# Kernel tuning notes

Hardware: AMD Instinct MI355X
Metric: run time of the kernel (lower is better)

Reference implementation:

```python
import jax, jax.numpy as jnp
import numpy as np

N = 50000      # nodes
E = 800000     # edges
F = 128        # node feature dim
H = 256        # hidden dim
A = 32         # action dim
G = 50         # graphs in batch
EPS = 1e-5     # batchnorm eps


def setup_inputs() -> dict:
    key = jax.random.key(0)
    ks = jax.random.split(key, 24)
    s = 0.02
    inp = {
        "x": jax.random.normal(ks[0], (N, F), jnp.float32),
        "edge_index": jax.random.randint(ks[1], (2, E), 0, N, jnp.int64),
        "batch": jnp.sort(jax.random.randint(ks[2], (N,), 0, G, jnp.int64)),
        "actions": jax.random.normal(ks[3], (A,), jnp.float32),
        # GCNConv weights (x @ W + b convention)
        "W1": jax.random.normal(ks[4], (F, H), jnp.float32) * s,
        "b1": jnp.zeros((H,), jnp.float32),
        "W2": jax.random.normal(ks[5], (H, H), jnp.float32) * s,
        "b2": jnp.zeros((H,), jnp.float32),
        "W3": jax.random.normal(ks[6], (H, H), jnp.float32) * s,
        "b3": jnp.zeros((H,), jnp.float32),
        # batchnorm affine params
        "g1": jnp.ones((H,), jnp.float32), "be1": jnp.zeros((H,), jnp.float32),
        "g2": jnp.ones((H,), jnp.float32), "be2": jnp.zeros((H,), jnp.float32),
        "g3": jnp.ones((H,), jnp.float32), "be3": jnp.zeros((H,), jnp.float32),
        # MLP head
        "fW1": jax.random.normal(ks[7], (H + A, H), jnp.float32) * s,
        "fb1": jnp.zeros((H,), jnp.float32),
        "fW2": jax.random.normal(ks[8], (H, H // 2), jnp.float32) * s,
        "fb2": jnp.zeros((H // 2,), jnp.float32),
        "fW3": jax.random.normal(ks[9], (H // 2, 1), jnp.float32) * s,
        "fb3": jnp.zeros((1,), jnp.float32),
    }
    return inp


def _batchnorm(h, gamma, beta):
    # training-mode batchnorm over the row dimension (biased variance, as torch)
    mu = h.mean(0)
    var = ((h - mu) ** 2).mean(0)
    return (h - mu) * jax.lax.rsqrt(var + EPS) * gamma + beta


def reference(x, edge_index, batch, actions,
              W1, b1, W2, b2, W3, b3,
              g1, be1, g2, be2, g3, be3,
              fW1, fb1, fW2, fb2, fW3, fb3):
    src, dst = edge_index[0], edge_index[1]
    n = x.shape[0]
    # GCN symmetric normalization with self-loops: deg_i = 1 + in_degree(i)
    deg = jnp.zeros((n,), x.dtype).at[dst].add(1.0) + 1.0
    dis = jax.lax.rsqrt(deg)                       # deg^{-1/2}
    enorm = dis[src] * dis[dst]                    # [E]
    self_norm = (dis * dis)[:, None]               # 1/deg_i for self-loop edge

    def gcn(h, W, b):
        h = h @ W                                  # [n,H]
        agg = jax.ops.segment_sum(h[src] * enorm[:, None], dst, num_segments=n)
        return agg + h * self_norm + b

    h = _batchnorm(jax.nn.relu(gcn(x, W1, b1)), g1, be1)   # dropout: identity (eval)
    h = _batchnorm(jax.nn.relu(gcn(h, W2, b2)), g2, be2)
    h = jax.nn.relu(gcn(h, W3, b3))

    # global_mean_pool
    counts = jax.ops.segment_sum(jnp.ones((n,), h.dtype), batch, num_segments=G)
    pooled = jax.ops.segment_sum(h, batch, num_segments=G) / jnp.maximum(counts, 1.0)[:, None]

    a = jnp.broadcast_to(actions[None, :], (G, actions.shape[0]))
    z = jnp.concatenate([pooled, a], axis=1)
    z = jax.nn.relu(z @ fW1 + fb1)
    z = _batchnorm(z, g3, be3)
    z = jax.nn.relu(z @ fW2 + fb2)
    return z @ fW3 + fb3                           # [G,1]
```

## Files before the change

kernel.cpp:

```cpp
#include <hip/hip_runtime.h>

#define NN 50000
#define NP1 (NN + 1)
#define NE 800000
#define FD 128
#define HD 256
#define AD 32
#define GN 50
#define BN_EPS 1e-5f

typedef float f32x4 __attribute__((ext_vector_type(4)));
typedef short s16x8 __attribute__((ext_vector_type(8)));

__device__ inline unsigned short f2bf(float f) {
    unsigned u = __float_as_uint(f);
    u += 0x7FFF + ((u >> 16) & 1);
    return (unsigned short)(u >> 16);
}
__device__ inline float bflo(unsigned u) { return __uint_as_float(u << 16); }
__device__ inline float bfhi(unsigned u) { return __uint_as_float(u & 0xffff0000u); }


__global__ void k_deg(const int* __restrict__ dst, int* __restrict__ counts) {
    int e = blockIdx.x * blockDim.x + threadIdx.x;
    if (e < NE) atomicAdd(&counts[dst[e]], 1);
}

__global__ void k_dis(const int* __restrict__ counts, float* __restrict__ dis) {
    int i = blockIdx.x * blockDim.x + threadIdx.x;
    if (i < NN) dis[i] = rsqrtf(1.0f + (float)counts[i]);
    if (i == 0) dis[NN] = 0.0f;
}

__global__ void k_scan1(const int* __restrict__ counts, int* __restrict__ rowptr,
                        int* __restrict__ bsum) {
    __shared__ int s[1024];
    int t = threadIdx.x;
    int i = blockIdx.x * 1024 + t;
    int v = (i < NN) ? ((counts[i] + 1) & ~1) : 0;
    s[t] = v;
    __syncthreads();
    for (int off = 1; off < 1024; off <<= 1) {
        int u = (t >= off) ? s[t - off] : 0;
        __syncthreads();
        s[t] += u;
        __syncthreads();
    }
    if (i < NN) rowptr[i + 1] = s[t];
    if (t == 1023) bsum[blockIdx.x] = s[1023];
}

__global__ void k_scan2(int* __restrict__ bsum, int* __restrict__ rowptr, int nblk) {
    if (threadIdx.x == 0 && blockIdx.x == 0) {
        int run = 0;
        for (int b = 0; b < nblk; ++b) { int t = bsum[b]; bsum[b] = run; run += t; }
        rowptr[0] = 0;
    }
}

__global__ void k_scan3(int* __restrict__ rowptr, const int* __restrict__ bsum) {
    int i = blockIdx.x * blockDim.x + threadIdx.x;
    if (i < NN) rowptr[i + 1] += bsum[i >> 10];
}

__global__ void k_csr(const int* __restrict__ src, const int* __restrict__ dst,
                      const int* __restrict__ rowptr, int* __restrict__ fill,
                      unsigned short* __restrict__ csru) {
    int e = blockIdx.x * blockDim.x + threadIdx.x;
    if (e < NE) {
        int d = dst[e];
        int p = rowptr[d] + atomicAdd(&fill[d], 1);
        csru[p] = (unsigned short)src[e];
    }
}

__global__ void k_pad(const int* __restrict__ counts, const int* __restrict__ rowptr,
                      unsigned short* __restrict__ csru) {
    int n = blockIdx.x * 256 + threadIdx.x;
    if (n < NN) {
        int c = counts[n];
        if (c & 1) csru[rowptr[n] + c] = (unsigned short)NN;
    }
}

__global__ void k_dsum(const int* __restrict__ rowptr, const unsigned short* __restrict__ csru,
                       const float* __restrict__ dis, float* __restrict__ dsum) {
    int n = blockIdx.x * 256 + threadIdx.x;
    if (n < NN) {
        float s = dis[n];
        int e1 = rowptr[n + 1];
        for (int e = rowptr[n]; e < e1; ++e) s += dis[csru[e]];
        dsum[n] = s;
    }
}


__global__ void k_castW(const float* __restrict__ W, unsigned short* __restrict__ Wt, int K) {
    int idx = blockIdx.x * 256 + threadIdx.x;
    if (idx < K * HD) {
        int c = idx / K, k = idx - c * K;
        Wt[idx] = f2bf(W[(size_t)k * HD + c]);
    }
}

__global__ void k_castx(const float* __restrict__ x, const float* __restrict__ dis,
                        unsigned* __restrict__ xb) {
    int idx = blockIdx.x * 256 + threadIdx.x;
    if (idx < NN * (FD / 2)) {
        int n = idx >> 6, jj = idx & 63;
        int chunk = jj >> 4, w = jj & 15;
        float sc = dis[n];
        float2 v = *(const float2*)&x[(size_t)n * FD + jj * 2];
        xb[((size_t)chunk * NP1 + n) * 16 + w] =
            ((unsigned)f2bf(v.y * sc) << 16) | f2bf(v.x * sc);
    }
}

__global__ void k_zrow(unsigned* __restrict__ xb, unsigned* __restrict__ tbuf) {
    int t = threadIdx.x;
    if (t < 64) xb[((size_t)(t >> 4) * NP1 + NN) * 16 + (t & 15)] = 0;
    else if (t < 192) {
        int q = t - 64;
        tbuf[((size_t)(q >> 4) * NP1 + NN) * 16 + (q & 15)] = 0;
    }
}


template<int K>
__global__ __launch_bounds__(256) void k_mms(const unsigned* __restrict__ Ab,
                                             const unsigned short* __restrict__ Wt,
                                             const float* __restrict__ bias,
                                             const float* __restrict__ dis,
                                             unsigned short* __restrict__ Cout,
                                             float* __restrict__ stats8) {
    __shared__ __align__(16) short Als[128 * 40];
    __shared__ __align__(16) short Bls[256 * 40];
    int t = threadIdx.x;
    int rowBase = blockIdx.x * 128;
    int wid = t >> 6, lane = t & 63;
    int lr = lane & 15, kg = (lane >> 4) * 8;

    f32x4 acc[2][16];
#pragma unroll
    for (int i = 0; i < 2; ++i)
#pragma unroll
        for (int j = 0; j < 16; ++j) acc[i][j] = (f32x4){0.f, 0.f, 0.f, 0.f};

    for (int k0 = 0; k0 < K; k0 += 32) {
        const unsigned* ap = Ab + (size_t)(k0 >> 5) * NP1 * 16;
#pragma unroll
        for (int it = 0; it < 2; ++it) {
            int task = t + it * 256;
            int row = task >> 2, k8 = (task & 3) * 8;
            int grow = rowBase + row;
            s16x8 v = (s16x8)(short)0;
            if (grow < NN)
                v = *(const s16x8*)&ap[grow * 16 + (task & 3) * 4];
            *(s16x8*)&Als[row * 40 + k8] = v;
        }
#pragma unroll
        for (int it = 0; it < 4; ++it) {
            int task = t + it * 256;
            int col = task >> 2, k8 = (task & 3) * 8;
            *(s16x8*)&Bls[col * 40 + k8] = *(const s16x8*)&Wt[(size_t)col * K + k0 + k8];
        }
        __syncthreads();
        s16x8 a0 = *(const s16x8*)&Als[(wid * 32 + lr) * 40 + kg];
        s16x8 a1 = *(const s16x8*)&Als[(wid * 32 + 16 + lr) * 40 + kg];
#pragma unroll
        for (int nf = 0; nf < 16; ++nf) {
            s16x8 b = *(const s16x8*)&Bls[(nf * 16 + lr) * 40 + kg];
            acc[0][nf] = __builtin_amdgcn_mfma_f32_16x16x32_bf16(a0, b, acc[0][nf], 0, 0, 0);
            acc[1][nf] = __builtin_amdgcn_mfma_f32_16x16x32_bf16(a1, b, acc[1][nf], 0, 0, 0);
        }
        __syncthreads();
    }

    int r4 = (lane >> 4) * 4;
    bool okr[2][4];
    float scr[2][4];
#pragma unroll
    for (int mf = 0; mf < 2; ++mf)
#pragma unroll
        for (int r = 0; r < 4; ++r) {
            int row = rowBase + wid * 32 + mf * 16 + r4 + r;
            okr[mf][r] = row < NN;
            scr[mf][r] = (row < NN) ? dis[row] : 1.0f;
        }

    float* ps = (float*)Als;
    float* pq = (float*)Bls;
#pragma unroll
    for (int nf = 0; nf < 16; ++nf) {
        int col = nf * 16 + lr;
        float bcol = bias[col];
        float s_ = 0.f, q_ = 0.f;
#pragma unroll
        for (int mf = 0; mf < 2; ++mf)
#pragma unroll
            for (int r = 0; r < 4; ++r) {
                float vv = okr[mf][r] ? fmaxf(acc[mf][nf][r] + bcol, 0.f) : 0.f;
                s_ += vv;
                q_ = fmaf(vv, vv, q_);
                if (okr[mf][r]) {
                    int row = rowBase + wid * 32 + mf * 16 + r4 + r;
                    Cout[((size_t)(col >> 5) * NP1 + row) * 32 + (col & 31)]
                        = f2bf(vv * scr[mf][r]);
                }
            }
        s_ += __shfl_xor(s_, 16); s_ += __shfl_xor(s_, 32);
        q_ += __shfl_xor(q_, 16); q_ += __shfl_xor(q_, 32);
        if (lane < 16) { ps[wid * 256 + col] = s_; pq[wid * 256 + col] = q_; }
    }
    __syncthreads();
    float ssum = ps[t] + ps[256 + t] + ps[512 + t] + ps[768 + t];
    float qsum = pq[t] + pq[256 + t] + pq[512 + t] + pq[768 + t];
    float* sb = stats8 + (size_t)(blockIdx.x & 7) * 2 * HD;
    atomicAdd(&sb[t], ssum);
    atomicAdd(&sb[HD + t], qsum);
}


template<int K>
__global__ __launch_bounds__(256) void k_mmp(const unsigned* __restrict__ Ab,
                                             const unsigned short* __restrict__ Wt,
                                             const float* __restrict__ bias,
                                             const int* __restrict__ batch,
                                             const int* __restrict__ gstart,
                                             float* __restrict__ pooled) {
    __shared__ __align__(16) short Als[128 * 40];
    __shared__ __align__(16) short Bls[256 * 40];
    int t = threadIdx.x;
    int rowBase = blockIdx.x * 128;
    int wid = t >> 6, lane = t & 63;
    int lr = lane & 15, kg = (lane >> 4) * 8;

    f32x4 acc[2][16];
#pragma unroll
    for (int i = 0; i < 2; ++i)
#pragma unroll
        for (int j = 0; j < 16; ++j) acc[i][j] = (f32x4){0.f, 0.f, 0.f, 0.f};

    for (int k0 = 0; k0 < K; k0 += 32) {
        const unsigned* ap = Ab + (size_t)(k0 >> 5) * NP1 * 16;
#pragma unroll
        for (int it = 0; it < 2; ++it) {
            int task = t + it * 256;
            int row = task >> 2, k8 = (task & 3) * 8;
            int grow = rowBase + row;
            s16x8 v = (s16x8)(short)0;
            if (grow < NN)
                v = *(const s16x8*)&ap[grow * 16 + (task & 3) * 4];
            *(s16x8*)&Als[row * 40 + k8] = v;
        }
#pragma unroll
        for (int it = 0; it < 4; ++it) {
            int task = t + it * 256;
            int col = task >> 2, k8 = (task & 3) * 8;
            *(s16x8*)&Bls[col * 40 + k8] = *(const s16x8*)&Wt[(size_t)col * K + k0 + k8];
        }
        __syncthreads();
        s16x8 a0 = *(const s16x8*)&Als[(wid * 32 + lr) * 40 + kg];
        s16x8 a1 = *(const s16x8*)&Als[(wid * 32 + 16 + lr) * 40 + kg];
#pragma unroll
        for (int nf = 0; nf < 16; ++nf) {
            s16x8 b = *(const s16x8*)&Bls[(nf * 16 + lr) * 40 + kg];
            acc[0][nf] = __builtin_amdgcn_mfma_f32_16x16x32_bf16(a0, b, acc[0][nf], 0, 0, 0);
            acc[1][nf] = __builtin_amdgcn_mfma_f32_16x16x32_bf16(a1, b, acc[1][nf], 0, 0, 0);
        }
        __syncthreads();
    }

    int r4 = (lane >> 4) * 4;
    int nvalid = NN - rowBase;
    int lastRow = rowBase + (nvalid < 128 ? nvalid : 128) - 1;
    int gA = batch[rowBase];
    int gB = batch[lastRow];
    float* ps = (float*)Bls;
    int slot = wid * 4 + (lane >> 4);

    if (gB - gA <= 1) {
        int split = (gB > gA) ? gstart[gB] : (rowBase + 128);
#pragma unroll
        for (int nf = 0; nf < 16; ++nf) {
            int col = nf * 16 + lr;
            float bcol = bias[col];
            float s_ = 0.f;
#pragma unroll
            for (int mf = 0; mf < 2; ++mf)
#pragma unroll
                for (int r = 0; r < 4; ++r) {
                    int row = rowBase + wid * 32 + mf * 16 + r4 + r;
                    float vv = fmaxf(acc[mf][nf][r] + bcol, 0.f);
                    s_ += (row < NN && row < split) ? vv : 0.f;
                }
            ps[slot * 256 + col] = s_;
        }
        __syncthreads();
        {
            float tot = 0.f;
#pragma unroll
            for (int s = 0; s < 16; ++s) tot += ps[s * 256 + t];
            atomicAdd(&pooled[gA * HD + t], tot);
        }
        if (gB > gA) {
            __syncthreads();
#pragma unroll
            for (int nf = 0; nf < 16; ++nf) {
                int col = nf * 16 + lr;
                float bcol = bias[col];
                float s_ = 0.f;
#pragma unroll
                for (int mf = 0; mf < 2; ++mf)
#pragma unroll
                    for (int r = 0; r < 4; ++r) {
                        int row = rowBase + wid * 32 + mf * 16 + r4 + r;
                        float vv = fmaxf(acc[mf][nf][r] + bcol, 0.f);
                        s_ += (row < NN && row >= split) ? vv : 0.f;
                    }
                ps[slot * 256 + col] = s_;
            }
            __syncthreads();
            float tot = 0.f;
#pragma unroll
            for (int s = 0; s < 16; ++s) tot += ps[s * 256 + t];
            atomicAdd(&pooled[gB * HD + t], tot);
        }
    } else {
#pragma unroll
        for (int mf = 0; mf < 2; ++mf)
#pragma unroll
            for (int r = 0; r < 4; ++r) {
                int row = rowBase + wid * 32 + mf * 16 + r4 + r;
                if (row < NN) {
                    int g = batch[row];
#pragma unroll
                    for (int nf = 0; nf < 16; ++nf) {
                        int col = nf * 16 + lr;
                        float vv = fmaxf(acc[mf][nf][r] + bias[col], 0.f);
                        atomicAdd(&pooled[g * HD + col], vv);
                    }
                }
            }
    }
}


template<int NCHUNK, bool AFFINE>
__global__ __launch_bounds__(256) void k_aggc(const unsigned* __restrict__ tin,
                                              const int* __restrict__ rowptr,
                                              const unsigned short* __restrict__ csru,
                                              const float* __restrict__ dis,
                                              const float* __restrict__ aff_a,
                                              const float* __restrict__ aff_c,
                                              const float* __restrict__ dsum,
                                              unsigned* __restrict__ outp) {
    int c = blockIdx.x & (NCHUNK - 1);
    int g = blockIdx.x / NCHUNK;
    int local = threadIdx.x >> 4;
    int jj = threadIdx.x & 15;
    int n = g * 16 + local;
    if (n >= NN) return;
    const unsigned* tc = tin + (size_t)c * NP1 * 16;
    unsigned u0 = tc[n * 16 + jj];
    float acc0 = bflo(u0), acc1 = bfhi(u0);
    int e0 = rowptr[n], e1 = rowptr[n + 1];
    int e = e0;
    for (; e + 8 <= e1; e += 8) {
        const unsigned* p32 = (const unsigned*)(csru + e);
        unsigned i01 = p32[0], i23 = p32[1], i45 = p32[2], i67 = p32[3];
        unsigned v0 = tc[(i01 & 0xffffu) * 16 + jj];
        unsigned v1 = tc[(i01 >> 16) * 16 + jj];
        unsigned v2 = tc[(i23 & 0xffffu) * 16 + jj];
        unsigned v3 = tc[(i23 >> 16) * 16 + jj];
        unsigned v4 = tc[(i45 & 0xffffu) * 16 + jj];
        unsigned v5 = tc[(i45 >> 16) * 16 + jj];
        unsigned v6 = tc[(i67 & 0xffffu) * 16 + jj];
        unsigned v7 = tc[(i67 >> 16) * 16 + jj];
        acc0 += bflo(v0); acc1 += bfhi(v0);
        acc0 += bflo(v1); acc1 += bfhi(v1);
        acc0 += bflo(v2); acc1 += bfhi(v2);
        acc0 += bflo(v3); acc1 += bfhi(v3);
        acc0 += bflo(v4); acc1 += bfhi(v4);
        acc0 += bflo(v5); acc1 += bfhi(v5);
        acc0 += bflo(v6); acc1 += bfhi(v6);
        acc0 += bflo(v7); acc1 += bfhi(v7);
    }
    for (; e < e1; e += 2) {
        unsigned i01 = *(const unsigned*)(csru + e);
        unsigned v0 = tc[(i01 & 0xffffu) * 16 + jj];
        unsigned v1 = tc[(i01 >> 16) * 16 + jj];
        acc0 += bflo(v0) + bflo(v1);
        acc1 += bfhi(v0) + bfhi(v1);
    }
    float dn = dis[n];
    if (AFFINE) {
        float wn = dsum[n];
        int col2 = c * 16 + jj;
        float2 a2 = *(const float2*)&aff_a[2 * col2];
        float2 c2 = *(const float2*)&aff_c[2 * col2];
        acc0 = dn * fmaf(a2.x, acc0, c2.x * wn);
        acc1 = dn * fmaf(a2.y, acc1, c2.y * wn);
    } else {
        acc0 *= dn;
        acc1 *= dn;
    }
    outp[((size_t)c * NP1 + n) * 16 + jj] = ((unsigned)f2bf(acc1) << 16) | f2bf(acc0);
}


__global__ void k_affine(const float* __restrict__ stats8, const float* __restrict__ g,
                         const float* __restrict__ be, float* __restrict__ a,
                         float* __restrict__ c) {
    int j = threadIdx.x;
    float s = 0.f, q = 0.f;
    for (int b = 0; b < 8; ++b) {
        s += stats8[(size_t)b * 2 * HD + j];
        q += stats8[(size_t)b * 2 * HD + HD + j];
    }
    float mu = s * (1.0f / NN);
    float var = q * (1.0f / NN) - mu * mu;
    float rs = rsqrtf(var + BN_EPS);
    float aj = g[j] * rs;
    a[j] = aj;
    c[j] = be[j] - mu * aj;
}


__global__ void k_bounds(const int* __restrict__ batch, int* __restrict__ gstart) {
    int g = threadIdx.x;
    if (g <= GN) {
        int lo = 0, hi = NN;
        while (lo < hi) {
            int mid = (lo + hi) >> 1;
            if (batch[mid] < g) lo = mid + 1; else hi = mid;
        }
        gstart[g] = lo;
    }
}

__global__ void k_poolfin(float* __restrict__ pooled, const int* __restrict__ gstart) {
    int idx = blockIdx.x * blockDim.x + threadIdx.x;
    if (idx < GN * HD) {
        int g = idx >> 8;
        float c = (float)max(gstart[g + 1] - gstart[g], 1);
        pooled[idx] /= c;
    }
}


__global__ __launch_bounds__(256) void k_head1(const float* __restrict__ pooled,
                                               const float* __restrict__ actions,
                                               const float* __restrict__ fW1,
                                               const float* __restrict__ fb1,
                                               float* __restrict__ z1) {
    int g = blockIdx.x, j = threadIdx.x;
    float acc = fb1[j];
    for (int k = 0; k < HD; ++k)
        acc = fmaf(pooled[g * HD + k], fW1[k * HD + j], acc);
    for (int k = 0; k < AD; ++k)
        acc = fmaf(actions[k], fW1[(HD + k) * HD + j], acc);
    z1[g * HD + j] = fmaxf(acc, 0.f);
}

__global__ __launch_bounds__(256) void k_headbn(float* __restrict__ z1,
                                                const float* __restrict__ g3,
                                                const float* __restrict__ be3) {
    int j = threadIdx.x;
    float s = 0.f, q = 0.f;
    for (int g = 0; g < GN; ++g) {
        float v = z1[g * HD + j];
        s += v;
        q = fmaf(v, v, q);
    }
    float mu = s * (1.0f / GN);
    float var = q * (1.0f / GN) - mu * mu;
    float rs = rsqrtf(var + BN_EPS);
    float ga = g3[j], be = be3[j];
    for (int g = 0; g < GN; ++g)
        z1[g * HD + j] = fmaf((z1[g * HD + j] - mu) * rs, ga, be);
}

__global__ __launch_bounds__(128) void k_head2(const float* __restrict__ z1,
                                               const float* __restrict__ fW2,
                                               const float* __restrict__ fb2,
                                               float* __restrict__ z2) {
    int g = blockIdx.x, j = threadIdx.x;
    float acc = fb2[j];
    for (int k = 0; k < HD; ++k)
        acc = fmaf(z1[g * HD + k], fW2[k * (HD / 2) + j], acc);
    z2[g * (HD / 2) + j] = fmaxf(acc, 0.f);
}

__global__ __launch_bounds__(64) void k_head3(const float* __restrict__ z2,
                                              const float* __restrict__ fW3,
                                              const float* __restrict__ fb3,
                                              float* __restrict__ out) {
    int g = threadIdx.x;
    if (g < GN) {
        float acc = fb3[0];
        for (int k = 0; k < HD / 2; ++k)
            acc = fmaf(z2[g * (HD / 2) + k], fW3[k], acc);
        out[g] = acc;
    }
}


static inline size_t align256(size_t x) { return (x + 255) & ~(size_t)255; }

extern "C" void kernel_launch(void* const* d_in, const int* in_sizes, int n_in,
                              void* d_out, int out_size, void* d_ws, size_t ws_size,
                              hipStream_t stream) {
    const float* x       = (const float*)d_in[0];
    const int*   ei      = (const int*)d_in[1];
    const int*   batch   = (const int*)d_in[2];
    const float* actions = (const float*)d_in[3];
    const float* W1 = (const float*)d_in[4];
    const float* b1 = (const float*)d_in[5];
    const float* W2 = (const float*)d_in[6];
    const float* b2 = (const float*)d_in[7];
    const float* W3 = (const float*)d_in[8];
    const float* b3 = (const float*)d_in[9];
    const float* g1  = (const float*)d_in[10];
    const float* be1 = (const float*)d_in[11];
    const float* g2  = (const float*)d_in[12];
    const float* be2 = (const float*)d_in[13];
    const float* g3  = (const float*)d_in[14];
    const float* be3 = (const float*)d_in[15];
    const float* fW1 = (const float*)d_in[16];
    const float* fb1 = (const float*)d_in[17];
    const float* fW2 = (const float*)d_in[18];
    const float* fb2 = (const float*)d_in[19];
    const float* fW3 = (const float*)d_in[20];
    const float* fb3 = (const float*)d_in[21];
    float* out = (float*)d_out;

    const int* esrc = ei;
    const int* edst = ei + NE;

    char* p = (char*)d_ws;
    size_t off = 0;
    auto carve = [&](size_t bytes) { void* r = p + off; off = align256(off + bytes); return r; };
    unsigned* xb   = (unsigned*)carve((size_t)4 * NP1 * 16 * 4);
    unsigned* xa   = (unsigned*)carve((size_t)4 * NP1 * 16 * 4);
    unsigned* tbuf = (unsigned*)carve((size_t)8 * NP1 * 16 * 4);
    unsigned* ah   = (unsigned*)carve((size_t)8 * NP1 * 16 * 4);
    float* dis     = (float*)carve((size_t)NP1 * 4);
    int*   counts  = (int*)carve((size_t)NN * 4);
    int*   rowptr  = (int*)carve((size_t)(NN + 1) * 4);
    int*   fill    = (int*)carve((size_t)NN * 4);
    unsigned short* csru = (unsigned short*)carve((size_t)(NE + NN) * 2);
    float* dsum    = (float*)carve((size_t)NN * 4);
    int*   bsum    = (int*)carve(64 * 4);
    float* pooled  = (float*)carve((size_t)GN * HD * 4);
    int*   gstart  = (int*)carve((size_t)(GN + 1) * 4);
    float* stats8  = (float*)carve((size_t)8 * 2 * HD * 4);
    float* affa    = (float*)carve(HD * 4);
    float* affc    = (float*)carve(HD * 4);
    float* z1      = (float*)carve((size_t)GN * HD * 4);
    float* z2      = (float*)carve((size_t)GN * (HD / 2) * 4);
    unsigned short* W1t = (unsigned short*)carve((size_t)FD * HD * 2);
    unsigned short* W2t = (unsigned short*)carve((size_t)HD * HD * 2);
    unsigned short* W3t = (unsigned short*)carve((size_t)HD * HD * 2);
    (void)ws_size;

    const int TB = 256;
    const int ebk = (NE + TB - 1) / TB;
    const int nbk = (NN + TB - 1) / TB;
    const int scanblk = (NN + 1023) / 1024;
    const int mmg = (NN + 127) / 128;
    const int ngrp = NN / 16;

    k_castW<<<(FD * HD + 255) / 256, 256, 0, stream>>>(W1, W1t, FD);
    k_castW<<<(HD * HD + 255) / 256, 256, 0, stream>>>(W2, W2t, HD);
    k_castW<<<(HD * HD + 255) / 256, 256, 0, stream>>>(W3, W3t, HD);

    hipMemsetAsync(counts, 0, (size_t)NN * 4, stream);
    k_deg<<<ebk, TB, 0, stream>>>(edst, counts);
    k_dis<<<nbk, TB, 0, stream>>>(counts, dis);
    k_scan1<<<scanblk, 1024, 0, stream>>>(counts, rowptr, bsum);
    k_scan2<<<1, 64, 0, stream>>>(bsum, rowptr, scanblk);
    k_scan3<<<nbk, TB, 0, stream>>>(rowptr, bsum);
    hipMemsetAsync(fill, 0, (size_t)NN * 4, stream);
    k_csr<<<ebk, TB, 0, stream>>>(esrc, edst, rowptr, fill, csru);
    k_pad<<<nbk, TB, 0, stream>>>(counts, rowptr, csru);
    k_dsum<<<nbk, TB, 0, stream>>>(rowptr, csru, dis, dsum);
    k_bounds<<<1, 64, 0, stream>>>(batch, gstart);

    k_castx<<<(NN * (FD / 2) + 255) / 256, 256, 0, stream>>>(x, dis, xb);
    k_zrow<<<1, 192, 0, stream>>>(xb, tbuf);

    hipMemsetAsync(stats8, 0, (size_t)8 * 2 * HD * 4, stream);
    k_aggc<4, false><<<4 * ngrp, TB, 0, stream>>>(xb, rowptr, csru, dis,
                                                  nullptr, nullptr, nullptr, xa);
    k_mms<FD><<<mmg, TB, 0, stream>>>(xa, W1t, b1, dis, (unsigned short*)tbuf, stats8);
    k_affine<<<1, HD, 0, stream>>>(stats8, g1, be1, affa, affc);

    hipMemsetAsync(stats8, 0, (size_t)8 * 2 * HD * 4, stream);
    k_aggc<8, true><<<8 * ngrp, TB, 0, stream>>>(tbuf, rowptr, csru, dis,
                                                 affa, affc, dsum, ah);
    k_mms<HD><<<mmg, TB, 0, stream>>>(ah, W2t, b2, dis, (unsigned short*)tbuf, stats8);
    k_affine<<<1, HD, 0, stream>>>(stats8, g2, be2, affa, affc);

    hipMemsetAsync(pooled, 0, (size_t)GN * HD * 4, stream);
    k_aggc<8, true><<<8 * ngrp, TB, 0, stream>>>(tbuf, rowptr, csru, dis,
                                                 affa, affc, dsum, ah);
    k_mmp<HD><<<mmg, TB, 0, stream>>>(ah, W3t, b3, batch, gstart, pooled);

    k_poolfin<<<(GN * HD + TB - 1) / TB, TB, 0, stream>>>(pooled, gstart);

    k_head1<<<GN, TB, 0, stream>>>(pooled, actions, fW1, fb1, z1);
    k_headbn<<<1, TB, 0, stream>>>(z1, g3, be3);
    k_head2<<<GN, 128, 0, stream>>>(z1, fW2, fb2, z2);
    k_head3<<<1, 64, 0, stream>>>(z2, fW3, fb3, out);
}
```

Measured before the change: 430.4 us.

## Sort nodes by degree for balanced aggregation and widen per-thread gathers

Adds a single-block counting sort that orders nodes by in-degree, and the aggregation kernel now processes nodes in that permuted order so that neighboring threads in a wavefront have similar edge counts and diverge less. Each thread now handles 8 bytes (two packed bf16 pairs) per neighbor instead of 4, so 8 threads cover a 64-byte chunk row and a block covers 32 nodes. The cost is an extra serial single-block sort kernel, plus scattered output writes and lost locality from the permuted node order.

```diff
diff --git a/kernel.cpp b/kernel.cpp
--- a/kernel.cpp
+++ b/kernel.cpp
@@ -30,6 +30,35 @@
     int i = blockIdx.x * blockDim.x + threadIdx.x;
     if (i < NN) dis[i] = rsqrtf(1.0f + (float)counts[i]);
     if (i == 0) dis[NN] = 0.0f;
+}
+
+__global__ __launch_bounds__(1024) void k_sort(const int* __restrict__ counts,
+                                               int* __restrict__ perm) {
+    __shared__ int hist[256];
+    __shared__ int scan[256];
+    __shared__ int boff[256];
+    __shared__ int fill[256];
+    int t = threadIdx.x;
+    if (t < 256) hist[t] = 0;
+    __syncthreads();
+    for (int i = t; i < NN; i += 1024)
+        atomicAdd(&hist[min(counts[i], 255)], 1);
+    __syncthreads();
+    if (t < 256) scan[t] = hist[t];
+    __syncthreads();
+    for (int off = 1; off < 256; off <<= 1) {
+        int v = (t < 256 && t >= off) ? scan[t - off] : 0;
+        __syncthreads();
+        if (t < 256) scan[t] += v;
+        __syncthreads();
+    }
+    if (t < 256) { boff[t] = scan[t] - hist[t]; fill[t] = 0; }
+    __syncthreads();
+    for (int i = t; i < NN; i += 1024) {
+        int b = min(counts[i], 255);
+        int pos = boff[b] + atomicAdd(&fill[b], 1);
+        perm[pos] = i;
+    }
 }
 
 __global__ void k_scan1(const int* __restrict__ counts, int* __restrict__ rowptr,
@@ -347,65 +376,73 @@
 
 
 template<int NCHUNK, bool AFFINE>
-__global__ __launch_bounds__(256) void k_aggc(const unsigned* __restrict__ tin,
+__global__ __launch_bounds__(256) void k_aggs(const unsigned* __restrict__ tin,
                                               const int* __restrict__ rowptr,
                                               const unsigned short* __restrict__ csru,
                                               const float* __restrict__ dis,
+                                              const int* __restrict__ perm,
                                               const float* __restrict__ aff_a,
                                               const float* __restrict__ aff_c,
                                               const float* __restrict__ dsum,
                                               unsigned* __restrict__ outp) {
     int c = blockIdx.x & (NCHUNK - 1);
     int g = blockIdx.x / NCHUNK;
-    int local = threadIdx.x >> 4;
-    int jj = threadIdx.x & 15;
-    int n = g * 16 + local;
-    if (n >= NN) return;
+    int local = threadIdx.x >> 3;
+    int jj2 = threadIdx.x & 7;
+    int i = g * 32 + local;
+    if (i >= NN) return;
+    int n = perm[i];
     const unsigned* tc = tin + (size_t)c * NP1 * 16;
-    unsigned u0 = tc[n * 16 + jj];
-    float acc0 = bflo(u0), acc1 = bfhi(u0);
+    uint2 u0 = *(const uint2*)&tc[n * 16 + jj2 * 2];
+    float a00 = bflo(u0.x), a01 = bfhi(u0.x);
+    float a10 = bflo(u0.y), a11 = bfhi(u0.y);
     int e0 = rowptr[n], e1 = rowptr[n + 1];
     int e = e0;
     for (; e + 8 <= e1; e += 8) {
         const unsigned* p32 = (const unsigned*)(csru + e);
         unsigned i01 = p32[0], i23 = p32[1], i45 = p32[2], i67 = p32[3];
-        unsigned v0 = tc[(i01 & 0xffffu) * 16 + jj];
-        unsigned v1 = tc[(i01 >> 16) * 16 + jj];
-        unsigned v2 = tc[(i23 & 0xffffu) * 16 + jj];
-        unsigned v3 = tc[(i23 >> 16) * 16 + jj];
-        unsigned v4 = tc[(i45 & 0xffffu) * 16 + jj];
-        unsigned v5 = tc[(i45 >> 16) * 16 + jj];
-        unsigned v6 = tc[(i67 & 0xffffu) * 16 + jj];
-        unsigned v7 = tc[(i67 >> 16) * 16 + jj];
-        acc0 += bflo(v0); acc1 += bfhi(v0);
-        acc0 += bflo(v1); acc1 += bfhi(v1);
-        acc0 += bflo(v2); acc1 += bfhi(v2);
-        acc0 += bflo(v3); acc1 += bfhi(v3);
-        acc0 += bflo(v4); acc1 += bfhi(v4);
-        acc0 += bflo(v5); acc1 += bfhi(v5);
-        acc0 += bflo(v6); acc1 += bfhi(v6);
-        acc0 += bflo(v7); acc1 += bfhi(v7);
+        uint2 v0 = *(const uint2*)&tc[(i01 & 0xffffu) * 16 + jj2 * 2];
+        uint2 v1 = *(const uint2*)&tc[(i01 >> 16) * 16 + jj2 * 2];
+        uint2 v2 = *(const uint2*)&tc[(i23 & 0xffffu) * 16 + jj2 * 2];
+        uint2 v3 = *(const uint2*)&tc[(i23 >> 16) * 16 + jj2 * 2];
+        uint2 v4 = *(const uint2*)&tc[(i45 & 0xffffu) * 16 + jj2 * 2];
+        uint2 v5 = *(const uint2*)&tc[(i45 >> 16) * 16 + jj2 * 2];
+        uint2 v6 = *(const uint2*)&tc[(i67 & 0xffffu) * 16 + jj2 * 2];
+        uint2 v7 = *(const uint2*)&tc[(i67 >> 16) * 16 + jj2 * 2];
+        a00 += bflo(v0.x); a01 += bfhi(v0.x); a10 += bflo(v0.y); a11 += bfhi(v0.y);
+        a00 += bflo(v1.x); a01 += bfhi(v1.x); a10 += bflo(v1.y); a11 += bfhi(v1.y);
+        a00 += bflo(v2.x); a01 += bfhi(v2.x); a10 += bflo(v2.y); a11 += bfhi(v2.y);
+        a00 += bflo(v3.x); a01 += bfhi(v3.x); a10 += bflo(v3.y); a11 += bfhi(v3.y);
+        a00 += bflo(v4.x); a01 += bfhi(v4.x); a10 += bflo(v4.y); a11 += bfhi(v4.y);
+        a00 += bflo(v5.x); a01 += bfhi(v5.x); a10 += bflo(v5.y); a11 += bfhi(v5.y);
+        a00 += bflo(v6.x); a01 += bfhi(v6.x); a10 += bflo(v6.y); a11 += bfhi(v6.y);
+        a00 += bflo(v7.x); a01 += bfhi(v7.x); a10 += bflo(v7.y); a11 += bfhi(v7.y);
     }
     for (; e < e1; e += 2) {
         unsigned i01 = *(const unsigned*)(csru + e);
-        unsigned v0 = tc[(i01 & 0xffffu) * 16 + jj];
-        unsigned v1 = tc[(i01 >> 16) * 16 + jj];
-        acc0 += bflo(v0) + bflo(v1);
-        acc1 += bfhi(v0) + bfhi(v1);
+        uint2 v0 = *(const uint2*)&tc[(i01 & 0xffffu) * 16 + jj2 * 2];
+        uint2 v1 = *(const uint2*)&tc[(i01 >> 16) * 16 + jj2 * 2];
+        a00 += bflo(v0.x) + bflo(v1.x); a01 += bfhi(v0.x) + bfhi(v1.x);
+        a10 += bflo(v0.y) + bflo(v1.y); a11 += bfhi(v0.y) + bfhi(v1.y);
     }
     float dn = dis[n];
+    float r00, r01, r10, r11;
     if (AFFINE) {
         float wn = dsum[n];
-        int col2 = c * 16 + jj;
-        float2 a2 = *(const float2*)&aff_a[2 * col2];
-        float2 c2 = *(const float2*)&aff_c[2 * col2];
-        acc0 = dn * fmaf(a2.x, acc0, c2.x * wn);
-        acc1 = dn * fmaf(a2.y, acc1, c2.y * wn);
+        int cb = c * 32 + jj2 * 4;
+        f32x4 a4 = *(const f32x4*)&aff_a[cb];
+        f32x4 c4 = *(const f32x4*)&aff_c[cb];
+        r00 = dn * fmaf(a4.x, a00, c4.x * wn);
+        r01 = dn * fmaf(a4.y, a01, c4.y * wn);
+        r10 = dn * fmaf(a4.z, a10, c4.z * wn);
+        r11 = dn * fmaf(a4.w, a11, c4.w * wn);
     } else {
-        acc0 *= dn;
-        acc1 *= dn;
-    }
-    outp[((size_t)c * NP1 + n) * 16 + jj] = ((unsigned)f2bf(acc1) << 16) | f2bf(acc0);
+        r00 = a00 * dn; r01 = a01 * dn; r10 = a10 * dn; r11 = a11 * dn;
+    }
+    uint2 o;
+    o.x = ((unsigned)f2bf(r01) << 16) | f2bf(r00);
+    o.y = ((unsigned)f2bf(r11) << 16) | f2bf(r10);
+    *(uint2*)&outp[((size_t)c * NP1 + n) * 16 + jj2 * 2] = o;
 }
 
 
@@ -549,6 +586,7 @@
     int*   counts  = (int*)carve((size_t)NN * 4);
     int*   rowptr  = (int*)carve((size_t)(NN + 1) * 4);
     int*   fill    = (int*)carve((size_t)NN * 4);
+    int*   perm    = (int*)carve((size_t)NN * 4);
     unsigned short* csru = (unsigned short*)carve((size_t)(NE + NN) * 2);
     float* dsum    = (float*)carve((size_t)NN * 4);
     int*   bsum    = (int*)carve(64 * 4);
@@ -569,7 +607,7 @@
     const int nbk = (NN + TB - 1) / TB;
     const int scanblk = (NN + 1023) / 1024;
     const int mmg = (NN + 127) / 128;
-    const int ngrp = NN / 16;
+    const int ngrp32 = (NN + 31) / 32;
 
     k_castW<<<(FD * HD + 255) / 256, 256, 0, stream>>>(W1, W1t, FD);
     k_castW<<<(HD * HD + 255) / 256, 256, 0, stream>>>(W2, W2t, HD);
@@ -578,6 +616,7 @@
     hipMemsetAsync(counts, 0, (size_t)NN * 4, stream);
     k_deg<<<ebk, TB, 0, stream>>>(edst, counts);
     k_dis<<<nbk, TB, 0, stream>>>(counts, dis);
+    k_sort<<<1, 1024, 0, stream>>>(counts, perm);
     k_scan1<<<scanblk, 1024, 0, stream>>>(counts, rowptr, bsum);
     k_scan2<<<1, 64, 0, stream>>>(bsum, rowptr, scanblk);
     k_scan3<<<nbk, TB, 0, stream>>>(rowptr, bsum);
@@ -591,20 +630,20 @@
     k_zrow<<<1, 192, 0, stream>>>(xb, tbuf);
 
     hipMemsetAsync(stats8, 0, (size_t)8 * 2 * HD * 4, stream);
-    k_aggc<4, false><<<4 * ngrp, TB, 0, stream>>>(xb, rowptr, csru, dis,
-                                                  nullptr, nullptr, nullptr, xa);
+    k_aggs<4, false><<<4 * ngrp32, TB, 0, stream>>>(xb, rowptr, csru, dis, perm,
+                                                    nullptr, nullptr, nullptr, xa);
     k_mms<FD><<<mmg, TB, 0, stream>>>(xa, W1t, b1, dis, (unsigned short*)tbuf, stats8);
     k_affine<<<1, HD, 0, stream>>>(stats8, g1, be1, affa, affc);
 
     hipMemsetAsync(stats8, 0, (size_t)8 * 2 * HD * 4, stream);
-    k_aggc<8, true><<<8 * ngrp, TB, 0, stream>>>(tbuf, rowptr, csru, dis,
-                                                 affa, affc, dsum, ah);
+    k_aggs<8, true><<<8 * ngrp32, TB, 0, stream>>>(tbuf, rowptr, csru, dis, perm,
+                                                   affa, affc, dsum, ah);
     k_mms<HD><<<mmg, TB, 0, stream>>>(ah, W2t, b2, dis, (unsigned short*)tbuf, stats8);
     k_affine<<<1, HD, 0, stream>>>(stats8, g2, be2, affa, affc);
 
     hipMemsetAsync(pooled, 0, (size_t)GN * HD * 4, stream);
-    k_aggc<8, true><<<8 * ngrp, TB, 0, stream>>>(tbuf, rowptr, csru, dis,
-                                                 affa, affc, dsum, ah);
+    k_aggs<8, true><<<8 * ngrp32, TB, 0, stream>>>(tbuf, rowptr, csru, dis, perm,
+                                                   affa, affc, dsum, ah);
     k_mmp<HD><<<mmg, TB, 0, stream>>>(ah, W3t, b3, batch, gstart, pooled);
 
     k_poolfin<<<(GN * HD + TB - 1) / TB, TB, 0, stream>>>(pooled, gstart);
```

Result: slower. 458.7 us (+6.6%).
